# Optimization experiments

Measured on AMD Instinct MI355X. Metric: run time of the kernel, lower is better.

Reference implementation:

```python
import jax, jax.numpy as jnp
import numpy as np

NEG = -10000.0
MAX_SPAN_LEN = 30
TOP_LAMBDA = 0.4
NUM_CATS = 7
FFNN = 1024
HID = 1024
B, S = 2, 2048
MAX_K = int(S * TOP_LAMBDA)  # 819; static top-k size (input_masks are full)


def fc(x, W, b, g, beta):
    # FullyConnectedLayer: Linear -> GELU(exact) -> LayerNorm (dropout = identity in eval)
    h = jax.nn.gelu(x @ W.T + b, approximate=False)
    mu = jnp.mean(h, axis=-1, keepdims=True)
    var = jnp.var(h, axis=-1, keepdims=True)
    return (h - mu) / jnp.sqrt(var + 1e-5) * g + beta


def setup_inputs():
    key = jax.random.key(0)
    ks = iter(jax.random.split(key, 48))
    def rn(shape, scale=0.02):
        return jax.random.normal(next(ks), shape, jnp.float32) * scale
    NF = NUM_CATS * FFNN
    inp = {
        'input_emb': jax.random.normal(next(ks), (B, S, HID), jnp.float32),
        'input_masks': jnp.ones((B, S), jnp.int32),
        # start/end mention MLPs
        'sm_W': rn((FFNN, HID)), 'sm_b': jnp.zeros((FFNN,)), 'sm_g': jnp.ones((FFNN,)), 'sm_beta': jnp.zeros((FFNN,)),
        'em_W': rn((FFNN, HID)), 'em_b': jnp.zeros((FFNN,)), 'em_g': jnp.ones((FFNN,)), 'em_beta': jnp.zeros((FFNN,)),
        # mention start/end classifiers (Linear(F,1)) and s2e classifier
        'ms_w': rn((FFNN,)), 'ms_b': jnp.zeros(()),
        'me_w': rn((FFNN,)), 'me_b': jnp.zeros(()),
        's2e_W': rn((FFNN, FFNN)), 's2e_b': jnp.zeros((FFNN,)),
        # coref start/end all-category MLPs (output num_cats*ffnn)
        'cs_W': rn((NF, HID)), 'cs_b': jnp.zeros((NF,)), 'cs_g': jnp.ones((NF,)), 'cs_beta': jnp.zeros((NF,)),
        'ce_W': rn((NF, HID)), 'ce_b': jnp.zeros((NF,)), 'ce_g': jnp.ones((NF,)), 'ce_beta': jnp.zeros((NF,)),
        # per-category bilinear antecedent weights/biases
        'Ws2s': rn((NUM_CATS, FFNN, FFNN)), 'We2e': rn((NUM_CATS, FFNN, FFNN)),
        'Ws2e': rn((NUM_CATS, FFNN, FFNN)), 'We2s': rn((NUM_CATS, FFNN, FFNN)),
        'Bs2s': rn((NUM_CATS, FFNN)), 'Be2e': rn((NUM_CATS, FFNN)),
        'Bs2e': rn((NUM_CATS, FFNN)), 'Be2s': rn((NUM_CATS, FFNN)),
    }
    return inp


def reference(input_emb, input_masks, sm_W, sm_b, sm_g, sm_beta, em_W, em_b, em_g, em_beta,
              ms_w, ms_b, me_w, me_b, s2e_W, s2e_b, cs_W, cs_b, cs_g, cs_beta,
              ce_W, ce_b, ce_g, ce_beta, Ws2s, We2e, Ws2e, We2s, Bs2s, Be2e, Bs2e, Be2s):
    # --- mention scores ---
    s = fc(input_emb, sm_W, sm_b, sm_g, sm_beta)   # [B,S,F]
    e = fc(input_emb, em_W, em_b, em_g, em_beta)   # [B,S,F]
    sm = s @ ms_w + ms_b                            # [B,S]
    em = e @ me_w + me_b                            # [B,S]
    joint = jnp.einsum('bsf,btf->bst', s @ s2e_W.T + s2e_b, e)
    scores = joint + sm[:, :, None] + em[:, None, :]
    i = jnp.arange(S)
    band = ((i[None, :] >= i[:, None]) & (i[None, :] - i[:, None] < MAX_SPAN_LEN)).astype(scores.dtype)
    scores = scores + (1.0 - band) * NEG            # mask_tensor (additive)
    # --- top-k span pruning ---
    flat = scores.reshape(B, S * S)
    _, idx = jax.lax.top_k(flat, MAX_K)
    k = (jnp.sum(input_masks, axis=-1).astype(jnp.float32) * TOP_LAMBDA).astype(jnp.int32)
    span_mask = (jnp.arange(MAX_K)[None, :] < k[:, None]).astype(jnp.int32)  # [B,K]
    idx = idx * span_mask + (1 - span_mask) * (S * S - 1)
    idx = jnp.sort(idx, axis=-1)
    start_ids = idx // S
    end_ids = idx % S
    topk_scores = jnp.take_along_axis(flat, idx, axis=1)          # [B,K]
    pair_scores = topk_scores[:, :, None] + topk_scores[:, None, :]
    # --- per-category coref reps (gather then MLP) ---
    start_reps = jnp.take_along_axis(input_emb, start_ids[:, :, None], axis=1)  # [B,K,H]
    end_reps = jnp.take_along_axis(input_emb, end_ids[:, :, None], axis=1)
    a_s = fc(start_reps, cs_W, cs_b, cs_g, cs_beta).reshape(B, MAX_K, NUM_CATS, FFNN).transpose(0, 2, 1, 3)
    a_e = fc(end_reps, ce_W, ce_b, ce_g, ce_beta).reshape(B, MAX_K, NUM_CATS, FFNN).transpose(0, 2, 1, 3)
    # --- per-category bilinear antecedent scores ---
    def bil(x, W, y):
        return jnp.einsum('bnkf,nfg,bnlg->bnkl', x, W, y)
    logits = bil(a_s, Ws2s, a_s) + bil(a_e, We2e, a_e) + bil(a_s, Ws2e, a_e) + bil(a_e, We2s, a_s)
    biases = (jnp.einsum('bnkf,nf->bnk', a_s, Bs2s) + jnp.einsum('bnkf,nf->bnk', a_e, Be2e)
              + jnp.einsum('bnkf,nf->bnk', a_e, Bs2e) + jnp.einsum('bnkf,nf->bnk', a_s, Be2s))[:, :, None, :]
    coref = logits + biases                                        # [B,N,K,K]
    kk = jnp.arange(MAX_K)
    tril = (kk[None, :] < kk[:, None]).astype(coref.dtype)         # strictly-lower (diag=-1)
    mask = tril[None, None] * span_mask[:, None, None, :].astype(coref.dtype)
    coref = coref + (1.0 - mask) * NEG
    return coref + pair_scores[:, None]
```

## Files before the change

kernel.cpp:

```cpp
#include <hip/hip_runtime.h>
#include <hip/hip_bf16.h>
#include <math.h>

#define S_    2048
#define NC_   7
#define MAXK  819
#define NK    1024
#define KP    896
#define Z_    14
#define NEGV  (-10000.0f)

typedef __attribute__((ext_vector_type(8))) short bf16x8;
typedef __attribute__((ext_vector_type(4))) float f32x4;

#define CFENCE asm volatile("" ::: "memory")
#define BAR    do { CFENCE; __builtin_amdgcn_s_barrier(); CFENCE; } while (0)

__device__ __forceinline__ void gload_lds16(const void* g, void* l) {
  __builtin_amdgcn_global_load_lds((const __attribute__((address_space(1))) unsigned int*)g,
                                   (__attribute__((address_space(3))) unsigned int*)l, 16, 0, 0);
}

__device__ __forceinline__ float gelu_exact(float x) {
  return 0.5f * x * (1.0f + erff(x * 0.70710678118654752f));
}
__device__ __forceinline__ unsigned short f2bf(float x) {
  __hip_bfloat16 h = __float2bfloat16(x);
  return *(unsigned short*)&h;
}
__device__ __forceinline__ float bf2f(unsigned short u) {
  __hip_bfloat16 h; *(unsigned short*)&h = u;
  return __bfloat162float(h);
}

template<bool OBF16, int EPI, bool MERGE>
__global__ __launch_bounds__(512, 2) void k_gemm8(
    const __hip_bfloat16* __restrict__ A, const __hip_bfloat16* __restrict__ B,
    void* __restrict__ Cv, const float* __restrict__ bias1, const float* __restrict__ bias2,
    const float* __restrict__ tkv, const int* __restrict__ kvp,
    int K, int nbn, long strideA, long strideB, int bmod7, long strideC,
    int ldc, int Mstore, int Nstore)
{
  __shared__ __align__(16) char lds[2][65536];
  const int tid = threadIdx.x;
  const int z = blockIdx.z;
  const int nwg = gridDim.x;
  const int xcd = blockIdx.x & 7, loc = blockIdx.x >> 3;
  const int q = nwg >> 3, r = nwg & 7;
  const int wg = (xcd < r ? xcd * (q + 1) : r * (q + 1) + (xcd - r) * q) + loc;
  const int bm = wg / nbn, bn = wg % nbn;
  const int m0 = bm * 256, n0 = bn * 256;
  const __hip_bfloat16* pA = A + (long)z * strideA;
  const __hip_bfloat16* pB = B + (long)(bmod7 ? (z % 7) : z) * strideB;
  const int wave = tid >> 6, lane = tid & 63;
  const int wm = wave >> 2, wn = wave & 3;
  const int lr = lane & 15, kh = lane >> 4;
  const long Kb = (long)K * 2;

  f32x4 acc[8][4];
  #pragma unroll
  for (int i = 0; i < 8; ++i)
    #pragma unroll
    for (int j = 0; j < 4; ++j)
      #pragma unroll
      for (int rr = 0; rr < 4; ++rr) acc[i][j][rr] = 0.0f;

  auto stageHalf = [&](int bb, int isB, int rh, int kt) {
    const long kbyte = (long)kt * 128;
    const char* basep;
    if (isB) {
      basep = (const char*)pB + (long)(n0 + rh * 128) * Kb;
    } else if (MERGE) {
      int arow0 = m0 + rh * 128;
      int zb = (arow0 >= KP) ? 1 : 0;
      basep = (const char*)(A + (long)(z + NC_ * zb) * strideA)
              + (long)(arow0 - KP * zb) * Kb;
    } else {
      basep = (const char*)pA + (long)(m0 + rh * 128) * Kb;
    }
    #pragma unroll
    for (int j = 0; j < 2; ++j) {
      int off = j * 8192 + tid * 16;
      int row = off >> 7;
      int col = off & 127;
      int gc = col ^ (((rh * 128 + row) & 7) << 4);
      gload_lds16(basep + (long)row * Kb + kbyte + gc,
                  &lds[bb][isB * 32768 + (rh * 128 + row) * 128 + col]);
    }
  };
  auto readA = [&](int c, int g, int kk) -> bf16x8 {
    int row = wm * 128 + g * 16 + lr;
    int colb = kk * 64 + kh * 16;
    return *(const bf16x8*)&lds[c][row * 128 + (colb ^ ((row & 7) << 4))];
  };
  auto readB = [&](int c, int ni, int kk) -> bf16x8 {
    int row = wn * 64 + ni * 16 + lr;
    int colb = kk * 64 + kh * 16;
    return *(const bf16x8*)&lds[c][32768 + row * 128 + (colb ^ ((row & 7) << 4))];
  };
  auto mfma4 = [&](int g0, bf16x8* af, bf16x8* bfr) {
    __builtin_amdgcn_s_setprio(1);
    #pragma unroll
    for (int mi = 0; mi < 4; ++mi)
      #pragma unroll
      for (int ni = 0; ni < 4; ++ni)
        acc[g0 + mi][ni] = __builtin_amdgcn_mfma_f32_16x16x32_bf16(af[mi], bfr[ni], acc[g0 + mi][ni], 0, 0, 0);
    __builtin_amdgcn_s_setprio(0);
  };

  const int nt = K >> 6;
  stageHalf(0, 1, 0, 0);
  stageHalf(0, 1, 1, 0);
  stageHalf(0, 0, 0, 0);
  stageHalf(0, 0, 1, 0);
  if (nt > 1) { stageHalf(1, 1, 0, 1); asm volatile("s_waitcnt vmcnt(2)" ::: "memory"); }
  else        { asm volatile("s_waitcnt vmcnt(0)" ::: "memory"); }
  BAR;
// ... 20 lines not shown
    #pragma unroll
    for (int i = 0; i < 4; ++i) a0f[i] = readA(c, i, 1);
    if (t + 1 < nt) stageHalf(cn, 0, 1, t + 1);
    BAR;
    mfma4(0, a0f, bfr);
    BAR;
    #pragma unroll
    for (int i = 0; i < 4; ++i) a1f[i] = readA(c, 4 + i, 1);
    if (t + 2 < nt) { stageHalf(c, 1, 0, t + 2); asm volatile("s_waitcnt vmcnt(2)" ::: "memory"); }
    else            { asm volatile("s_waitcnt vmcnt(0)" ::: "memory"); }
    BAR;
    mfma4(4, a1f, bfr);
    BAR;
  }

  const long coff = (long)z * strideC;
  int kval = 0, bb_ = 0;
  if (EPI == 2) { bb_ = z / NC_; kval = kvp[bb_]; }
  #pragma unroll
  for (int mi = 0; mi < 8; ++mi) {
    #pragma unroll
    for (int ni = 0; ni < 4; ++ni) {
      int n = n0 + wn * 64 + ni * 16 + lr;
      if (n >= Nstore) continue;
      float badd = 0.f;
      if (EPI == 0) { if (bias1) badd = bias1[n]; }
      if (EPI == 1) badd = (n >= 1024) ? bias2[n - 1024] : bias1[n];
      if (EPI == 2) badd = bias1[z * NK + n] + tkv[bb_ * NK + n];
      #pragma unroll
      for (int rr = 0; rr < 4; ++rr) {
        int m = m0 + wm * 128 + mi * 16 + kh * 4 + rr;
        if (m >= Mstore) continue;
        float v = acc[mi][ni][rr] + badd;
        long co; int mrow;
        if (MERGE) {
          int zb = (m >= KP) ? 1 : 0;
          co = (long)(z + NC_ * zb) * strideC;
          mrow = m - KP * zb;
        } else { co = coff; mrow = m; }
        if (EPI == 2) {
          v += tkv[bb_ * NK + m];
          if (!(n < m && n < kval)) v += NEGV;
        }
        if (OBF16) ((__hip_bfloat16*)Cv)[co + (long)mrow * ldc + n] = __float2bfloat16(v);
        else       ((float*)Cv)[co + (long)mrow * ldc + n] = v;
      }
    }
  }
}

template<int EPI>
__global__ __launch_bounds__(512, 1) void k_gemm44(
    const __hip_bfloat16* __restrict__ A, const __hip_bfloat16* __restrict__ B,
    float* __restrict__ Cv, const float* __restrict__ bias1, const float* __restrict__ bias2,
    int K, int nbn, int ldc, int Mstore, int Nstore)
{
  __shared__ __align__(16) char lds[3][49152];
  const int tid = threadIdx.x;
  const int nwg = gridDim.x;
  const int xcd = blockIdx.x & 7, loc = blockIdx.x >> 3;
  const int q = nwg >> 3, r = nwg & 7;
  const int wg = (xcd < r ? xcd * (q + 1) : r * (q + 1) + (xcd - r) * q) + loc;
  const int bm = wg / nbn, bn = wg % nbn;
  const int m0 = bm * 128, n0 = bn * 256;
  const int wave = tid >> 6, lane = tid & 63;
  const int wm = wave >> 2, wn = wave & 3;
  const int lr = lane & 15, kh = lane >> 4;
  const long Kb = (long)K * 2;

  f32x4 acc[4][4];
  #pragma unroll
  for (int i = 0; i < 4; ++i)
    #pragma unroll
    for (int j = 0; j < 4; ++j)
      #pragma unroll
      for (int rr = 0; rr < 4; ++rr) acc[i][j][rr] = 0.0f;

  auto stageA = [&](int bb, int kt) {
    const long kbyte = (long)kt * 128;
    const char* basep = (const char*)A + (long)m0 * Kb;
    #pragma unroll
    for (int j = 0; j < 2; ++j) {
      int off = j * 8192 + tid * 16;
      int row = off >> 7, col = off & 127;
      int gc = col ^ ((row & 7) << 4);
      gload_lds16(basep + (long)row * Kb + kbyte + gc, &lds[bb][row * 128 + col]);
    }
  };
  auto stageB = [&](int bb, int kt, int rh) {
    const long kbyte = (long)kt * 128;
    const char* basep = (const char*)B + (long)(n0 + rh * 128) * Kb;
    #pragma unroll
    for (int j = 0; j < 2; ++j) {
      int off = j * 8192 + tid * 16;
      int row = off >> 7, col = off & 127;
      int gc = col ^ (((rh * 128 + row) & 7) << 4);
      gload_lds16(basep + (long)row * Kb + kbyte + gc,
                  &lds[bb][16384 + (rh * 128 + row) * 128 + col]);
    }
  };
  auto readA = [&](int c, int g, int kk) -> bf16x8 {
    int row = wm * 64 + g * 16 + lr;
    int colb = kk * 64 + kh * 16;
    return *(const bf16x8*)&lds[c][row * 128 + (colb ^ ((row & 7) << 4))];
  };
  auto readB = [&](int c, int ni, int kk) -> bf16x8 {
    int row = wn * 64 + ni * 16 + lr;
    int colb = kk * 64 + kh * 16;
    return *(const bf16x8*)&lds[c][16384 + row * 128 + (colb ^ ((row & 7) << 4))];
  };
  auto mfmaAll = [&](bf16x8* af, bf16x8* bfr) {
    __builtin_amdgcn_s_setprio(1);
    #pragma unroll
    for (int mi = 0; mi < 4; ++mi)
      #pragma unroll
      for (int ni = 0; ni < 4; ++ni)
        acc[mi][ni] = __builtin_amdgcn_mfma_f32_16x16x32_bf16(af[mi], bfr[ni], acc[mi][ni], 0, 0, 0);
    __builtin_amdgcn_s_setprio(0);
  };

  const int nt = K >> 6;
  stageA(0, 0); stageB(0, 0, 0); stageB(0, 0, 1);
  if (nt > 1) { stageA(1, 1); stageB(1, 1, 0); stageB(1, 1, 1);
                asm volatile("s_waitcnt vmcnt(6)" ::: "memory"); }
  else        { asm volatile("s_waitcnt vmcnt(0)" ::: "memory"); }
  BAR;

  bf16x8 af[4], bfr[4];
  int ct = 0;
  for (int t = 0; t < nt; ++t) {
    const int b2 = (ct + 2 >= 3) ? ct - 1 : ct + 2;
    #pragma unroll
    for (int i = 0; i < 4; ++i) bfr[i] = readB(ct, i, 0);
    #pragma unroll
    for (int i = 0; i < 4; ++i) af[i] = readA(ct, i, 0);
    if (t + 2 < nt) stageA(b2, t + 2);
    BAR;
    mfmaAll(af, bfr);
    BAR;
    #pragma unroll
    for (int i = 0; i < 4; ++i) bfr[i] = readB(ct, i, 1);
    #pragma unroll
    for (int i = 0; i < 4; ++i) af[i] = readA(ct, i, 1);
    if (t + 2 < nt) { stageB(b2, t + 2, 0); stageB(b2, t + 2, 1);
                      asm volatile("s_waitcnt vmcnt(6)" ::: "memory"); }
    else            { asm volatile("s_waitcnt vmcnt(0)" ::: "memory"); }
    BAR;
    mfmaAll(af, bfr);
    BAR;
    ct = (ct + 1 >= 3) ? 0 : ct + 1;
  }

  #pragma unroll
  for (int mi = 0; mi < 4; ++mi) {
    #pragma unroll
    for (int ni = 0; ni < 4; ++ni) {
      int n = n0 + wn * 64 + ni * 16 + lr;
      if (n >= Nstore) continue;
      float badd = 0.f;
      if (EPI == 0) { if (bias1) badd = bias1[n]; }
      if (EPI == 1) badd = (n >= 1024) ? bias2[n - 1024] : bias1[n];
      #pragma unroll
      for (int rr = 0; rr < 4; ++rr) {
        int m = m0 + wm * 64 + mi * 16 + kh * 4 + rr;
        if (m >= Mstore) continue;
        Cv[(long)m * ldc + n] = acc[mi][ni][rr] + badd;
      }
    }
  }
}

template<bool APAT>
__global__ __launch_bounds__(256) void k_packsplit3(const float* __restrict__ s1, long stride1,
                                                    const float* __restrict__ s2, int split,
                                                    __hip_bfloat16* __restrict__ dst) {
  long idx4 = ((long)blockIdx.x * 256 + threadIdx.x) * 4;
  int rrow = (int)(idx4 >> 10), c = (int)(idx4 & 1023);
  const float* src = (rrow < split) ? s1 + (long)rrow * stride1 + c
                                    : s2 + (long)(rrow - split) * 1024 + c;
  float4 v = *(const float4*)src;
  float f[4] = {v.x, v.y, v.z, v.w};
  unsigned short h[4], l4[4];
  #pragma unroll
  for (int i = 0; i < 4; ++i) {
    h[i] = f2bf(f[i]);
    l4[i] = f2bf(f[i] - bf2f(h[i]));
  }
  unsigned short* d = (unsigned short*)dst + (long)rrow * 3072;
  ushort4 hv = {h[0], h[1], h[2], h[3]};
  ushort4 lv = {l4[0], l4[1], l4[2], l4[3]};
// ... 1 lines not shown
  *(ushort4*)(d + 1024 + c) = APAT ? hv : lv;
  *(ushort4*)(d + 2048 + c) = APAT ? lv : hv;
}

__global__ __launch_bounds__(256) void k_cast4(const float* __restrict__ x,
                                               __hip_bfloat16* __restrict__ y, long n4) {
  long i = (long)blockIdx.x * 256 + threadIdx.x;
  if (i >= n4) return;
  float4 v = ((const float4*)x)[i];
  ushort4 o = {f2bf(v.x), f2bf(v.y), f2bf(v.z), f2bf(v.w)};
  ((ushort4*)y)[i] = o;
}

__global__ __launch_bounds__(256) void k_packBbig(const float* __restrict__ Ws2s,
                                                  const float* __restrict__ We2e,
                                                  const float* __restrict__ Ws2e,
                                                  const float* __restrict__ We2s,
                                                  __hip_bfloat16* __restrict__ dst) {
  long idx4 = ((long)blockIdx.x * 256 + threadIdx.x) * 4;
  long rowid = idx4 >> 11;
  int c = (int)(idx4 & 2047);
  int cat = (int)(rowid >> 11);
  int n = (int)(rowid & 2047);
  const float* src;
  if (n < 1024) src = (c < 1024) ? Ws2s + ((long)cat * 1024 + n) * 1024 + c
                                 : Ws2e + ((long)cat * 1024 + n) * 1024 + (c - 1024);
  else          src = (c < 1024) ? We2s + ((long)cat * 1024 + (n - 1024)) * 1024 + c
                                 : We2e + ((long)cat * 1024 + (n - 1024)) * 1024 + (c - 1024);
  float4 v = *(const float4*)src;
  ushort4 o = {f2bf(v.x), f2bf(v.y), f2bf(v.z), f2bf(v.w)};
  *(ushort4*)((unsigned short*)dst + idx4) = o;
}

__global__ __launch_bounds__(256) void k_ln_s(const float* __restrict__ se,
                                              const float* __restrict__ g,
                                              const float* __restrict__ beta,
                                              const float* __restrict__ wv,
                                              const float* __restrict__ b0,
                                              float* __restrict__ smv,
                                              __hip_bfloat16* __restrict__ ssp) {
  int r = blockIdx.x;
  int c4 = threadIdx.x;
  float4 x = ((const float4*)(se + (long)r * 2048))[c4];
  float v[4] = {gelu_exact(x.x), gelu_exact(x.y), gelu_exact(x.z), gelu_exact(x.w)};
  float s = v[0] + v[1] + v[2] + v[3];
  float s2 = v[0]*v[0] + v[1]*v[1] + v[2]*v[2] + v[3]*v[3];
  __shared__ float red0[4], red1[4];
  for (int off = 32; off; off >>= 1) { s += __shfl_xor(s, off); s2 += __shfl_xor(s2, off); }
  int w = threadIdx.x >> 6;
  if ((threadIdx.x & 63) == 0) { red0[w] = s; red1[w] = s2; }
  __syncthreads();
  s  = red0[0] + red0[1] + red0[2] + red0[3];
  s2 = red1[0] + red1[1] + red1[2] + red1[3];
  float mu  = s / 1024.0f;
  float var = s2 / 1024.0f - mu * mu;
  float inv = 1.0f / sqrtf(var + 1e-5f);
  float4 gg = ((const float4*)g)[c4], bb = ((const float4*)beta)[c4];
  float y[4] = {(v[0]-mu)*inv*gg.x + bb.x, (v[1]-mu)*inv*gg.y + bb.y,
                (v[2]-mu)*inv*gg.z + bb.z, (v[3]-mu)*inv*gg.w + bb.w};
  float4 w4 = ((const float4*)wv)[c4];
  float d = y[0]*w4.x + y[1]*w4.y + y[2]*w4.z + y[3]*w4.w;
  for (int off = 32; off; off >>= 1) d += __shfl_xor(d, off);
  __syncthreads();
  if ((threadIdx.x & 63) == 0) red0[w] = d;
  __syncthreads();
  if (threadIdx.x == 0)
    smv[r] = red0[0] + red0[1] + red0[2] + red0[3] + b0[0];
  unsigned short h[4], l4[4];
  #pragma unroll
  for (int i = 0; i < 4; ++i) { h[i] = f2bf(y[i]); l4[i] = f2bf(y[i] - bf2f(h[i])); }
  ushort4 hv = {h[0], h[1], h[2], h[3]};
  ushort4 lv = {l4[0], l4[1], l4[2], l4[3]};
  unsigned short* dst = (unsigned short*)ssp + (long)r * 3072 + c4 * 4;
  *(ushort4*)dst          = hv;
  *(ushort4*)(dst + 1024) = hv;
  *(ushort4*)(dst + 2048) = lv;
}

__global__ __launch_bounds__(256) void k_ln_e(float* __restrict__ se,
                                              const float* __restrict__ g,
                                              const float* __restrict__ beta,
                                              const float* __restrict__ wv,
                                              const float* __restrict__ b0,
                                              float* __restrict__ emv) {
  int r = blockIdx.x;
  int c4 = threadIdx.x;
  float4* rowp = (float4*)(se + (long)r * 2048 + 1024);
  float4 x = rowp[c4];
  float v[4] = {gelu_exact(x.x), gelu_exact(x.y), gelu_exact(x.z), gelu_exact(x.w)};
  float s = v[0] + v[1] + v[2] + v[3];
  float s2 = v[0]*v[0] + v[1]*v[1] + v[2]*v[2] + v[3]*v[3];
  __shared__ float red0[4], red1[4];
  for (int off = 32; off; off >>= 1) { s += __shfl_xor(s, off); s2 += __shfl_xor(s2, off); }
  int w = threadIdx.x >> 6;
  if ((threadIdx.x & 63) == 0) { red0[w] = s; red1[w] = s2; }
  __syncthreads();
  s  = red0[0] + red0[1] + red0[2] + red0[3];
  s2 = red1[0] + red1[1] + red1[2] + red1[3];
  float mu  = s / 1024.0f;
  float var = s2 / 1024.0f - mu * mu;
  float inv = 1.0f / sqrtf(var + 1e-5f);
  float4 gg = ((const float4*)g)[c4], bb = ((const float4*)beta)[c4];
  float4 y = {(v[0]-mu)*inv*gg.x + bb.x, (v[1]-mu)*inv*gg.y + bb.y,
              (v[2]-mu)*inv*gg.z + bb.z, (v[3]-mu)*inv*gg.w + bb.w};
  float4 w4 = ((const float4*)wv)[c4];
  float d = y.x*w4.x + y.y*w4.y + y.z*w4.z + y.w*w4.w;
  for (int off = 32; off; off >>= 1) d += __shfl_xor(d, off);
  __syncthreads();
  if ((threadIdx.x & 63) == 0) red0[w] = d;
  __syncthreads();
  if (threadIdx.x == 0)
    emv[r] = red0[0] + red0[1] + red0[2] + red0[3] + b0[0];
  rowp[c4] = y;
}

__global__ __launch_bounds__(256) void k_gelu_ln_cats(const __hip_bfloat16* __restrict__ h,
                                                      const float* __restrict__ g,
                                                      const float* __restrict__ beta,
                                                      __hip_bfloat16* __restrict__ a_cat, int half) {
  int r = blockIdx.x;
  int b = (r >= KP) ? 1 : 0, k = r - KP * b;
  const ushort4* row = (const ushort4*)((const unsigned short*)h + (long)r * 7168);
  float v[28];
  float s = 0.f, s2 = 0.f;
  #pragma unroll
  for (int j = 0; j < 7; ++j) {
    ushort4 u = row[threadIdx.x + 256 * j];
    #pragma unroll
    for (int e = 0; e < 4; ++e) {
      float x = bf2f(((const unsigned short*)&u)[e]);
      float ge = gelu_exact(x);
      v[j * 4 + e] = ge; s += ge; s2 += ge * ge;
    }
  }
  __shared__ float red0[4], red1[4];
  for (int off = 32; off; off >>= 1) { s += __shfl_xor(s, off); s2 += __shfl_xor(s2, off); }
  int w = threadIdx.x >> 6;
  if ((threadIdx.x & 63) == 0) { red0[w] = s; red1[w] = s2; }
  __syncthreads();
  s  = red0[0] + red0[1] + red0[2] + red0[3];
  s2 = red1[0] + red1[1] + red1[2] + red1[3];
  float mu  = s / 7168.0f;
  float var = s2 / 7168.0f - mu * mu;
  float inv = 1.0f / sqrtf(var + 1e-5f);
  #pragma unroll
  for (int j = 0; j < 7; ++j) {
// ... 26 lines not shown
  for (int qq = 0; qq < 16; ++qq) sreg[qq] = sp[l + 64 * qq];
  float myS = smv[(b << 11) + s];
  if (l < 32) {
    int j = l;
    if (j >= 30 || s + j >= S_)
      band[((long)(b << 11) + s) * 32 + j] = -3.0e38f;
  }
  {
    const float* ep = se + ((long)(b << 11) + s0) * 2048 + 1024;
    ebuf[0][tid * 2]     = ep[tid * 2];
    ebuf[0][tid * 2 + 1] = ep[tid * 2 + 1];
  }
  for (int it = 0; it < 37; ++it) {
    int t = s0 + it;
    __syncthreads();
    if (it + 1 < 37 && s0 + it + 1 < S_) {
      const float* ep = se + ((long)(b << 11) + s0 + it + 1) * 2048 + 1024;
      ebuf[(it + 1) & 1][tid * 2]     = ep[tid * 2];
      ebuf[(it + 1) & 1][tid * 2 + 1] = ep[tid * 2 + 1];
    }
    int j = t - s;
    if (t < S_ && j >= 0 && j < 30) {
      const float* eb = ebuf[it & 1];
      float acc = 0.f;
      #pragma unroll
      for (int qq = 0; qq < 16; ++qq) acc += sreg[qq] * eb[l + 64 * qq];
      for (int off = 32; off; off >>= 1) acc += __shfl_xor(acc, off);
      if (l == 0)
        band[((long)(b << 11) + s) * 32 + j] = acc + myS + emv[(b << 11) + t];
    }
  }
}

__device__ __forceinline__ void bitonic1024(unsigned* buf) {
  int tid = threadIdx.x;
  __syncthreads();
  for (int k = 2; k <= 1024; k <<= 1)
    for (int j = k >> 1; j > 0; j >>= 1) {
      int ixj = tid ^ j;
      if (ixj > tid) {
        unsigned a = buf[tid], c = buf[ixj];
        bool up = ((tid & k) == 0);
        if (up ? (a > c) : (a < c)) { buf[tid] = c; buf[ixj] = a; }
      }
      __syncthreads();
    }
}

__global__ __launch_bounds__(1024) void k_topk(const float* __restrict__ band,
                                               const int* __restrict__ masks,
                                               int* __restrict__ starts, int* __restrict__ ends,
                                               float* __restrict__ tk, int* __restrict__ kvalid_out) {
  int b = blockIdx.x;
  const float* bb = band + (long)b * 65536;
  __shared__ unsigned hist[16][256];
  __shared__ int sh_digit, sh_R, sh_msum;
  __shared__ unsigned cntG, cntE;
  __shared__ unsigned listG[832];
  __shared__ unsigned listE[1024];
  __shared__ unsigned buf[1024];
  int tid = threadIdx.x;
  int wv = tid >> 6;

  if (tid == 0) sh_msum = 0;
  __syncthreads();
  int pm = masks[b * S_ + tid] + masks[b * S_ + 1024 + tid];
  atomicAdd(&sh_msum, pm);
  __syncthreads();
  int kv = (int)((float)sh_msum * 0.4f);
  if (kv > MAXK) kv = MAXK;

  unsigned prefix = 0;
  int R = kv;
  if (kv > 0) {
    for (int shift = 24; shift >= 0; shift -= 8) {
      for (int i = tid; i < 4096; i += 1024) ((unsigned*)hist)[i] = 0;
      __syncthreads();
      for (int i = tid; i < 65536; i += 1024) {
        unsigned u = __float_as_uint(bb[i]);
        unsigned key = (u & 0x80000000u) ? ~u : (u | 0x80000000u);
        bool ok = (shift == 24) || ((key >> (shift + 8)) == (prefix >> (shift + 8)));
        if (ok) atomicAdd(&hist[wv][(key >> shift) & 255u], 1u);
      }
      __syncthreads();
      if (tid < 256) {
        unsigned sacc = 0;
        #pragma unroll
        for (int ww = 0; ww < 16; ++ww) sacc += hist[ww][tid];
        hist[0][tid] = sacc;
      }
      __syncthreads();
      if (tid == 0) {
        unsigned cum = 0; int d;
        for (d = 255; d >= 0; --d) {
          unsigned hc = hist[0][d];
          if (cum + hc >= (unsigned)R) break;
          cum += hc;
        }
        if (d < 0) d = 0;
        sh_digit = d; sh_R = R - (int)cum;
      }
      __syncthreads();
      prefix |= ((unsigned)sh_digit) << shift;
      R = sh_R;
      __syncthreads();
    }
  }
  if (tid == 0) { cntG = 0; cntE = 0; }
  __syncthreads();
  if (kv > 0) {
    for (int i = tid; i < 65536; i += 1024) {
      unsigned u = __float_as_uint(bb[i]);
      unsigned key = (u & 0x80000000u) ? ~u : (u | 0x80000000u);
      if (key > prefix) { unsigned p = atomicAdd(&cntG, 1u); if (p < 832) listG[p] = (unsigned)i; }
      else if (key == prefix) { unsigned p = atomicAdd(&cntE, 1u); if (p < 1024) listE[p] = (unsigned)i; }
    }
  }
  __syncthreads();
  int nG = (int)cntG, nE = (int)cntE, need = R;
  buf[tid] = (tid < nE) ? listE[tid] : 0xFFFFFFFFu;
  bitonic1024(buf);
  if (tid < need) listG[nG + tid] = buf[tid];
  __syncthreads();
  unsigned v2 = (tid < (unsigned)kv) ? listG[tid] : 0xFFFFFFFFu;
  __syncthreads();
  buf[tid] = v2;
  bitonic1024(buf);
  {
    int s, t; float val;
    if (tid < kv) {
      unsigned i = buf[tid];
      s = (int)(i >> 5); t = s + (int)(i & 31);
      val = bb[i];
    } else {
      s = S_ - 1; t = S_ - 1;
      val = bb[(S_ - 1) * 32 + 0];
    }
    starts[b * NK + tid] = s;
    ends[b * NK + tid] = t;
    tk[b * NK + tid] = val;
  }
  if (tid == 0) kvalid_out[b] = kv;
}

__global__ __launch_bounds__(256) void k_gather(const float* __restrict__ emb,
                                                const int* __restrict__ starts,
                                                const int* __restrict__ ends,
                                                __hip_bfloat16* __restrict__ reps_s,
// ... 67 lines not shown
  const float* Ws2s = (const float*)d_in[24];
  const float* We2e = (const float*)d_in[25];
  const float* Ws2e = (const float*)d_in[26];
  const float* We2s = (const float*)d_in[27];
  const float* Bs2s = (const float*)d_in[28];
  const float* Be2e = (const float*)d_in[29];
  const float* Bs2e = (const float*)d_in[30];
  const float* Be2s = (const float*)d_in[31];
  float* outp = (float*)d_out;
  char* ws = (char*)d_ws;
  (void)in_sizes; (void)n_in; (void)out_size; (void)ws_size;

  const size_t o_embsp = 0;
  const size_t o_bse   = 25165824;
  const size_t o_ssp   = 0;
  const size_t o_s2W   = 25165824;
  const size_t o_repss = 0;
  const size_t o_repse = 4194304;
  const size_t o_csWb  = 8388608;
  const size_t o_ceWb  = 23068672;
  const size_t o_Bbig  = 0;
  const size_t o_se    = 37748736;
  const size_t o_s2    = 71303168;
  const size_t o_h     = 88080384;
  const size_t o_acat  = 146800640;
  const size_t o_smv   = 205520896;
  const size_t o_emv   = o_smv + 16384;
  const size_t o_band  = o_emv + 16384;
  const size_t o_starts= o_band + 524288;
  const size_t o_ends  = o_starts + 8192;
  const size_t o_tk    = o_ends + 8192;
  const size_t o_kv    = o_tk + 8192;
  const size_t o_biasv = o_kv + 256;

  __hip_bfloat16* embsp = (__hip_bfloat16*)(ws + o_embsp);
  __hip_bfloat16* bse   = (__hip_bfloat16*)(ws + o_bse);
  __hip_bfloat16* ssp   = (__hip_bfloat16*)(ws + o_ssp);
  __hip_bfloat16* s2Wsp = (__hip_bfloat16*)(ws + o_s2W);
  __hip_bfloat16* repss = (__hip_bfloat16*)(ws + o_repss);
  __hip_bfloat16* repse = (__hip_bfloat16*)(ws + o_repse);
  __hip_bfloat16* csWb  = (__hip_bfloat16*)(ws + o_csWb);
  __hip_bfloat16* ceWb  = (__hip_bfloat16*)(ws + o_ceWb);
  __hip_bfloat16* Bbig  = (__hip_bfloat16*)(ws + o_Bbig);
  float* se_buf = (float*)(ws + o_se);
  float* s2_buf = (float*)(ws + o_s2);
  __hip_bfloat16* h_buf = (__hip_bfloat16*)(ws + o_h);
  __hip_bfloat16* Vcat  = (__hip_bfloat16*)(ws + o_h);
  __hip_bfloat16* a_cat = (__hip_bfloat16*)(ws + o_acat);
  float* smv_p = (float*)(ws + o_smv);
  float* emv_p = (float*)(ws + o_emv);
  float* band_p = (float*)(ws + o_band);
  int* starts_p = (int*)(ws + o_starts);
  int* ends_p = (int*)(ws + o_ends);
  float* tk_p = (float*)(ws + o_tk);
  int* kv_p = (int*)(ws + o_kv);
  float* biasv_p = (float*)(ws + o_biasv);

  k_packsplit3<true ><<<4096, 256, 0, stream>>>(x_emb, 1024, x_emb, 4096, embsp);
  k_packsplit3<false><<<2048, 256, 0, stream>>>(smW, 1024, emW, 1024, bse);
  k_gemm44<1><<<dim3(256, 1, 1), 512, 0, stream>>>(embsp, bse, se_buf, smb, embb,
      3072, 8, 2048, 4096, 2048);
  k_ln_s<<<4096, 256, 0, stream>>>(se_buf, smg, smbe, msw, msb, smv_p, ssp);
  k_ln_e<<<4096, 256, 0, stream>>>(se_buf, emg, embe, mew, meb, emv_p);

  k_packsplit3<false><<<1024, 256, 0, stream>>>(s2eW, 1024, s2eW, 1024, s2Wsp);
  k_gemm44<0><<<dim3(128, 1, 1), 512, 0, stream>>>(ssp, s2Wsp, s2_buf, s2eb, nullptr,
      3072, 4, 1024, 4096, 1024);
  k_band<<<512, 512, 0, stream>>>(s2_buf, se_buf, smv_p, emv_p, band_p);

  k_topk<<<2, 1024, 0, stream>>>(band_p, masks, starts_p, ends_p, tk_p, kv_p);

  k_gather<<<2 * KP, 256, 0, stream>>>(x_emb, starts_p, ends_p, repss, repse);
  k_cast4<<<7168, 256, 0, stream>>>(csW, csWb, 1835008);
  k_cast4<<<7168, 256, 0, stream>>>(ceW, ceWb, 1835008);
  k_gemm8<true, 0, false><<<dim3(196, 1, 1), 512, 0, stream>>>(repss, csWb, h_buf, csb, nullptr,
      nullptr, nullptr, 1024, 28, 0, 0, 0, 0, 7168, 2 * KP, 7168);
  k_gelu_ln_cats<<<2 * KP, 256, 0, stream>>>(h_buf, csg, csbe, a_cat, 0);
  k_gemm8<true, 0, false><<<dim3(196, 1, 1), 512, 0, stream>>>(repse, ceWb, h_buf, ceb, nullptr,
      nullptr, nullptr, 1024, 28, 0, 0, 0, 0, 7168, 2 * KP, 7168);
  k_packBbig<<<28672, 256, 0, stream>>>(Ws2s, We2e, Ws2e, We2s, Bbig);
  k_gelu_ln_cats<<<2 * KP, 256, 0, stream>>>(h_buf, ceg, cebe, a_cat, 1);

  k_gemm8<true, 0, true><<<dim3(56, 1, NC_), 512, 0, stream>>>(a_cat, Bbig, Vcat, nullptr, nullptr,
      nullptr, nullptr, 2048, 8, (long)NK * 2048, (long)2048 * 2048, 0, (long)NK * 2048, 2048, 2 * KP, 2048);
  k_bias<<<(Z_ * KP) / 4, 256, 0, stream>>>(a_cat, Bs2s, Be2e, Bs2e, Be2s, biasv_p);
  k_gemm8<false, 2, false><<<dim3(16, 1, Z_), 512, 0, stream>>>(a_cat, Vcat, outp, biasv_p, nullptr,
      tk_p, kv_p, 2048, 4, (long)NK * 2048, (long)NK * 2048, 0, (long)MAXK * MAXK, MAXK, MAXK, MAXK);
}
```

Measured before the change: 747.9 us.

## Parallelize top-k selection, fuse start/end layernorms, retile s2e GEMM

Replaces the two-block radix top-k with a multi-block pipeline. A global histogram on the top 12 bits finds a threshold bin, a collect pass keeps only candidate indices, and the final radix refinement runs on that much smaller set. It also fuses the start and end LayerNorm kernels into one launch and gives the s2e GEMM a 128-wide N tile so it launches 256 workgroups. The merged-batch path of k_gemm8 is removed, and the V GEMM now runs per batch over z=14 padded to 1024 rows, which does extra work on padded rows. The new top-k adds several small launches and global atomics.

```diff
diff --git a/kernel.cpp b/kernel.cpp
--- a/kernel.cpp
+++ b/kernel.cpp
@@ -32,8 +32,12 @@
   __hip_bfloat16 h; *(unsigned short*)&h = u;
   return __bfloat162float(h);
 }
-
-template<bool OBF16, int EPI, bool MERGE>
+__device__ __forceinline__ unsigned fkey(float f) {
+  unsigned u = __float_as_uint(f);
+  return (u & 0x80000000u) ? ~u : (u | 0x80000000u);
+}
+
+template<bool OBF16, int EPI>
 __global__ __launch_bounds__(512, 2) void k_gemm8(
     const __hip_bfloat16* __restrict__ A, const __hip_bfloat16* __restrict__ B,
     void* __restrict__ Cv, const float* __restrict__ bias1, const float* __restrict__ bias2,
@@ -67,22 +71,12 @@
 
   auto stageHalf = [&](int bb, int isB, int rh, int kt) {
     const long kbyte = (long)kt * 128;
-    const char* basep;
-    if (isB) {
-      basep = (const char*)pB + (long)(n0 + rh * 128) * Kb;
-    } else if (MERGE) {
-      int arow0 = m0 + rh * 128;
-      int zb = (arow0 >= KP) ? 1 : 0;
-      basep = (const char*)(A + (long)(z + NC_ * zb) * strideA)
-              + (long)(arow0 - KP * zb) * Kb;
-    } else {
-      basep = (const char*)pA + (long)(m0 + rh * 128) * Kb;
-    }
+    const char* basep = isB ? (const char*)pB + (long)(n0 + rh * 128) * Kb
+                            : (const char*)pA + (long)(m0 + rh * 128) * Kb;
     #pragma unroll
     for (int j = 0; j < 2; ++j) {
       int off = j * 8192 + tid * 16;
-      int row = off >> 7;
-      int col = off & 127;
+      int row = off >> 7, col = off & 127;
       int gc = col ^ (((rh * 128 + row) & 7) << 4);
       gload_lds16(basep + (long)row * Kb + kbyte + gc,
                   &lds[bb][isB * 32768 + (rh * 128 + row) * 128 + col]);
@@ -169,47 +163,43 @@
         int m = m0 + wm * 128 + mi * 16 + kh * 4 + rr;
         if (m >= Mstore) continue;
         float v = acc[mi][ni][rr] + badd;
-        long co; int mrow;
-        if (MERGE) {
-          int zb = (m >= KP) ? 1 : 0;
-          co = (long)(z + NC_ * zb) * strideC;
-          mrow = m - KP * zb;
-        } else { co = coff; mrow = m; }
         if (EPI == 2) {
           v += tkv[bb_ * NK + m];
           if (!(n < m && n < kval)) v += NEGV;
         }
-        if (OBF16) ((__hip_bfloat16*)Cv)[co + (long)mrow * ldc + n] = __float2bfloat16(v);
-        else       ((float*)Cv)[co + (long)mrow * ldc + n] = v;
+        if (OBF16) ((__hip_bfloat16*)Cv)[coff + (long)m * ldc + n] = __float2bfloat16(v);
+        else       ((float*)Cv)[coff + (long)m * ldc + n] = v;
       }
     }
   }
 }
 
-template<int EPI>
+template<int EPI, int BN>
 __global__ __launch_bounds__(512, 1) void k_gemm44(
     const __hip_bfloat16* __restrict__ A, const __hip_bfloat16* __restrict__ B,
     float* __restrict__ Cv, const float* __restrict__ bias1, const float* __restrict__ bias2,
     int K, int nbn, int ldc, int Mstore, int Nstore)
 {
-  __shared__ __align__(16) char lds[3][49152];
+  constexpr int NI = BN / 64;
+  constexpr int NBH = BN / 128;
+  __shared__ __align__(16) char lds[3][16384 + BN * 128];
   const int tid = threadIdx.x;
   const int nwg = gridDim.x;
   const int xcd = blockIdx.x & 7, loc = blockIdx.x >> 3;
   const int q = nwg >> 3, r = nwg & 7;
   const int wg = (xcd < r ? xcd * (q + 1) : r * (q + 1) + (xcd - r) * q) + loc;
   const int bm = wg / nbn, bn = wg % nbn;
-  const int m0 = bm * 128, n0 = bn * 256;
+  const int m0 = bm * 128, n0 = bn * BN;
   const int wave = tid >> 6, lane = tid & 63;
   const int wm = wave >> 2, wn = wave & 3;
   const int lr = lane & 15, kh = lane >> 4;
   const long Kb = (long)K * 2;
 
-  f32x4 acc[4][4];
+  f32x4 acc[4][NI];
   #pragma unroll
   for (int i = 0; i < 4; ++i)
     #pragma unroll
-    for (int j = 0; j < 4; ++j)
+    for (int j = 0; j < NI; ++j)
       #pragma unroll
       for (int rr = 0; rr < 4; ++rr) acc[i][j][rr] = 0.0f;
 
@@ -242,7 +232,7 @@
     return *(const bf16x8*)&lds[c][row * 128 + (colb ^ ((row & 7) << 4))];
   };
   auto readB = [&](int c, int ni, int kk) -> bf16x8 {
-    int row = wn * 64 + ni * 16 + lr;
+    int row = wn * (NI * 16) + ni * 16 + lr;
     int colb = kk * 64 + kh * 16;
     return *(const bf16x8*)&lds[c][16384 + row * 128 + (colb ^ ((row & 7) << 4))];
   };
@@ -251,24 +241,32 @@
     #pragma unroll
     for (int mi = 0; mi < 4; ++mi)
       #pragma unroll
-      for (int ni = 0; ni < 4; ++ni)
+      for (int ni = 0; ni < NI; ++ni)
         acc[mi][ni] = __builtin_amdgcn_mfma_f32_16x16x32_bf16(af[mi], bfr[ni], acc[mi][ni], 0, 0, 0);
     __builtin_amdgcn_s_setprio(0);
   };
 
   const int nt = K >> 6;
-  stageA(0, 0); stageB(0, 0, 0); stageB(0, 0, 1);
-  if (nt > 1) { stageA(1, 1); stageB(1, 1, 0); stageB(1, 1, 1);
-                asm volatile("s_waitcnt vmcnt(6)" ::: "memory"); }
-  else        { asm volatile("s_waitcnt vmcnt(0)" ::: "memory"); }
+  stageA(0, 0);
+  #pragma unroll
+  for (int rh = 0; rh < NBH; ++rh) stageB(0, 0, rh);
+  if (nt > 1) {
+    stageA(1, 1);
+    #pragma unroll
+    for (int rh = 0; rh < NBH; ++rh) stageB(1, 1, rh);
+    if (BN == 256) asm volatile("s_waitcnt vmcnt(6)" ::: "memory");
+    else           asm volatile("s_waitcnt vmcnt(4)" ::: "memory");
+  } else {
+    asm volatile("s_waitcnt vmcnt(0)" ::: "memory");
+  }
   BAR;
 
-  bf16x8 af[4], bfr[4];
+  bf16x8 af[4], bfr[NI];
   int ct = 0;
   for (int t = 0; t < nt; ++t) {
     const int b2 = (ct + 2 >= 3) ? ct - 1 : ct + 2;
     #pragma unroll
-    for (int i = 0; i < 4; ++i) bfr[i] = readB(ct, i, 0);
+    for (int i = 0; i < NI; ++i) bfr[i] = readB(ct, i, 0);
     #pragma unroll
     for (int i = 0; i < 4; ++i) af[i] = readA(ct, i, 0);
     if (t + 2 < nt) stageA(b2, t + 2);
@@ -276,12 +274,17 @@
     mfmaAll(af, bfr);
     BAR;
     #pragma unroll
-    for (int i = 0; i < 4; ++i) bfr[i] = readB(ct, i, 1);
+    for (int i = 0; i < NI; ++i) bfr[i] = readB(ct, i, 1);
     #pragma unroll
     for (int i = 0; i < 4; ++i) af[i] = readA(ct, i, 1);
-    if (t + 2 < nt) { stageB(b2, t + 2, 0); stageB(b2, t + 2, 1);
-                      asm volatile("s_waitcnt vmcnt(6)" ::: "memory"); }
-    else            { asm volatile("s_waitcnt vmcnt(0)" ::: "memory"); }
+    if (t + 2 < nt) {
+      #pragma unroll
+      for (int rh = 0; rh < NBH; ++rh) stageB(b2, t + 2, rh);
+      if (BN == 256) asm volatile("s_waitcnt vmcnt(6)" ::: "memory");
+      else           asm volatile("s_waitcnt vmcnt(4)" ::: "memory");
+    } else {
+      asm volatile("s_waitcnt vmcnt(0)" ::: "memory");
+    }
     BAR;
     mfmaAll(af, bfr);
     BAR;
@@ -291,8 +294,8 @@
   #pragma unroll
   for (int mi = 0; mi < 4; ++mi) {
     #pragma unroll
-    for (int ni = 0; ni < 4; ++ni) {
-      int n = n0 + wn * 64 + ni * 16 + lr;
+    for (int ni = 0; ni < NI; ++ni) {
+      int n = n0 + wn * (NI * 16) + ni * 16 + lr;
       if (n >= Nstore) continue;
       float badd = 0.f;
       if (EPI == 0) { if (bias1) badd = bias1[n]; }
@@ -360,26 +363,32 @@
   *(ushort4*)((unsigned short*)dst + idx4) = o;
 }
 
-__global__ __launch_bounds__(256) void k_ln_s(const float* __restrict__ se,
-                                              const float* __restrict__ g,
-                                              const float* __restrict__ beta,
-                                              const float* __restrict__ wv,
-                                              const float* __restrict__ b0,
-                                              float* __restrict__ smv,
-                                              __hip_bfloat16* __restrict__ ssp) {
+__global__ __launch_bounds__(512) void k_ln_se(float* __restrict__ se,
+                                               const float* __restrict__ sg, const float* __restrict__ sbe,
+                                               const float* __restrict__ eg, const float* __restrict__ ebe,
+                                               const float* __restrict__ msw, const float* __restrict__ msb,
+                                               const float* __restrict__ mew, const float* __restrict__ meb,
+                                               float* __restrict__ smv, float* __restrict__ emv,
+                                               __hip_bfloat16* __restrict__ ssp) {
   int r = blockIdx.x;
-  int c4 = threadIdx.x;
-  float4 x = ((const float4*)(se + (long)r * 2048))[c4];
+  int tid = threadIdx.x;
+  int half = tid >> 8;
+  int c4 = tid & 255;
+  int w8 = tid >> 6;
+  const float* g    = half ? eg : sg;
+  const float* beta = half ? ebe : sbe;
+  const float* wv   = half ? mew : msw;
+  float4* rowp = (float4*)(se + (long)r * 2048 + half * 1024);
+  float4 x = rowp[c4];
   float v[4] = {gelu_exact(x.x), gelu_exact(x.y), gelu_exact(x.z), gelu_exact(x.w)};
   float s = v[0] + v[1] + v[2] + v[3];
   float s2 = v[0]*v[0] + v[1]*v[1] + v[2]*v[2] + v[3]*v[3];
-  __shared__ float red0[4], red1[4];
+  __shared__ float red0[8], red1[8];
   for (int off = 32; off; off >>= 1) { s += __shfl_xor(s, off); s2 += __shfl_xor(s2, off); }
-  int w = threadIdx.x >> 6;
-  if ((threadIdx.x & 63) == 0) { red0[w] = s; red1[w] = s2; }
-  __syncthreads();
-  s  = red0[0] + red0[1] + red0[2] + red0[3];
-  s2 = red1[0] + red1[1] + red1[2] + red1[3];
+  if ((tid & 63) == 0) { red0[w8] = s; red1[w8] = s2; }
+  __syncthreads();
+  s  = red0[half*4] + red0[half*4+1] + red0[half*4+2] + red0[half*4+3];
+  s2 = red1[half*4] + red1[half*4+1] + red1[half*4+2] + red1[half*4+3];
   float mu  = s / 1024.0f;
   float var = s2 / 1024.0f - mu * mu;
   float inv = 1.0f / sqrtf(var + 1e-5f);
@@ -390,56 +399,27 @@
   float d = y[0]*w4.x + y[1]*w4.y + y[2]*w4.z + y[3]*w4.w;
   for (int off = 32; off; off >>= 1) d += __shfl_xor(d, off);
   __syncthreads();
-  if ((threadIdx.x & 63) == 0) red0[w] = d;
-  __syncthreads();
-  if (threadIdx.x == 0)
-    smv[r] = red0[0] + red0[1] + red0[2] + red0[3] + b0[0];
-  unsigned short h[4], l4[4];
-  #pragma unroll
-  for (int i = 0; i < 4; ++i) { h[i] = f2bf(y[i]); l4[i] = f2bf(y[i] - bf2f(h[i])); }
-  ushort4 hv = {h[0], h[1], h[2], h[3]};
-  ushort4 lv = {l4[0], l4[1], l4[2], l4[3]};
-  unsigned short* dst = (unsigned short*)ssp + (long)r * 3072 + c4 * 4;
-  *(ushort4*)dst          = hv;
-  *(ushort4*)(dst + 1024) = hv;
-  *(ushort4*)(dst + 2048) = lv;
-}
-
-__global__ __launch_bounds__(256) void k_ln_e(float* __restrict__ se,
-                                              const float* __restrict__ g,
-                                              const float* __restrict__ beta,
-                                              const float* __restrict__ wv,
-                                              const float* __restrict__ b0,
-                                              float* __restrict__ emv) {
-  int r = blockIdx.x;
-  int c4 = threadIdx.x;
-  float4* rowp = (float4*)(se + (long)r * 2048 + 1024);
-  float4 x = rowp[c4];
-  float v[4] = {gelu_exact(x.x), gelu_exact(x.y), gelu_exact(x.z), gelu_exact(x.w)};
-  float s = v[0] + v[1] + v[2] + v[3];
-  float s2 = v[0]*v[0] + v[1]*v[1] + v[2]*v[2] + v[3]*v[3];
-  __shared__ float red0[4], red1[4];
-  for (int off = 32; off; off >>= 1) { s += __shfl_xor(s, off); s2 += __shfl_xor(s2, off); }
-  int w = threadIdx.x >> 6;
-  if ((threadIdx.x & 63) == 0) { red0[w] = s; red1[w] = s2; }
-  __syncthreads();
-  s  = red0[0] + red0[1] + red0[2] + red0[3];
-  s2 = red1[0] + red1[1] + red1[2] + red1[3];
-  float mu  = s / 1024.0f;
-  float var = s2 / 1024.0f - mu * mu;
-  float inv = 1.0f / sqrtf(var + 1e-5f);
-  float4 gg = ((const float4*)g)[c4], bb = ((const float4*)beta)[c4];
-  float4 y = {(v[0]-mu)*inv*gg.x + bb.x, (v[1]-mu)*inv*gg.y + bb.y,
-              (v[2]-mu)*inv*gg.z + bb.z, (v[3]-mu)*inv*gg.w + bb.w};
-  float4 w4 = ((const float4*)wv)[c4];
-  float d = y.x*w4.x + y.y*w4.y + y.z*w4.z + y.w*w4.w;
-  for (int off = 32; off; off >>= 1) d += __shfl_xor(d, off);
-  __syncthreads();
-  if ((threadIdx.x & 63) == 0) red0[w] = d;
-  __syncthreads();
-  if (threadIdx.x == 0)
-    emv[r] = red0[0] + red0[1] + red0[2] + red0[3] + b0[0];
-  rowp[c4] = y;
+  if ((tid & 63) == 0) red0[w8] = d;
+  __syncthreads();
+  if ((tid & 255) == 0) {
+    float dv = red0[half*4] + red0[half*4+1] + red0[half*4+2] + red0[half*4+3];
+    if (half == 0) smv[r] = dv + msb[0];
+    else           emv[r] = dv + meb[0];
+  }
+  if (half == 0) {
+    unsigned short h[4], l4[4];
+    #pragma unroll
+    for (int i = 0; i < 4; ++i) { h[i] = f2bf(y[i]); l4[i] = f2bf(y[i] - bf2f(h[i])); }
+    ushort4 hv = {h[0], h[1], h[2], h[3]};
+    ushort4 lv = {l4[0], l4[1], l4[2], l4[3]};
+    unsigned short* dst = (unsigned short*)ssp + (long)r * 3072 + c4 * 4;
+    *(ushort4*)dst          = hv;
+    *(ushort4*)(dst + 1024) = hv;
+    *(ushort4*)(dst + 2048) = lv;
+  } else {
+    float4 yo = {y[0], y[1], y[2], y[3]};
+    rowp[c4] = yo;
+  }
 }
 
 __global__ __launch_bounds__(256) void k_gelu_ln_cats(const __hip_bfloat16* __restrict__ h,
@@ -532,6 +512,103 @@
   }
 }
 
+__global__ __launch_bounds__(1024) void k_tkzero(unsigned* __restrict__ ghist,
+                                                 unsigned* __restrict__ gcnt) {
+  int i = blockIdx.x * 1024 + threadIdx.x;
+  if (i < 2 * 4096) ghist[i] = 0;
+  if (i < 2) gcnt[i] = 0;
+}
+
+__global__ __launch_bounds__(1024) void k_tkhist(const float* __restrict__ band,
+                                                 unsigned* __restrict__ ghist) {
+  int b = blockIdx.y;
+  const float* bb = band + (long)b * 65536;
+  __shared__ unsigned lh[4096];
+  int tid = threadIdx.x;
+  #pragma unroll
+  for (int j = 0; j < 4; ++j) lh[tid + j * 1024] = 0;
+  __syncthreads();
+  int base = blockIdx.x * 4096;
+  #pragma unroll
+  for (int j = 0; j < 4; ++j) {
+    unsigned key = fkey(bb[base + tid + j * 1024]);
+    atomicAdd(&lh[key >> 20], 1u);
+  }
+  __syncthreads();
+  #pragma unroll
+  for (int j = 0; j < 4; ++j) {
+    unsigned v = lh[tid + j * 1024];
+    if (v) atomicAdd(&ghist[b * 4096 + tid + j * 1024], v);
+  }
+}
+
+__global__ __launch_bounds__(1024) void k_tkscan(const unsigned* __restrict__ ghist,
+                                                 const int* __restrict__ masks,
+                                                 unsigned* __restrict__ sel) {
+  int b = blockIdx.x;
+  int tid = threadIdx.x;
+  __shared__ unsigned cs[1024];
+  __shared__ int red[16];
+  __shared__ int sh_kv;
+  int pm = masks[b * S_ + tid] + masks[b * S_ + 1024 + tid];
+  for (int off = 32; off; off >>= 1) pm += __shfl_xor(pm, off);
+  if ((tid & 63) == 0) red[tid >> 6] = pm;
+  __syncthreads();
+  if (tid == 0) {
+    int msum = 0;
+    for (int i = 0; i < 16; ++i) msum += red[i];
+    int kv = (int)((float)msum * 0.4f);
+    if (kv > MAXK) kv = MAXK;
+    sh_kv = kv;
+  }
+  __syncthreads();
+  int kv = sh_kv;
+  unsigned hbin[4];
+  unsigned ssum = 0;
+  #pragma unroll
+  for (int j = 0; j < 4; ++j) { hbin[j] = ghist[b * 4096 + tid * 4 + j]; ssum += hbin[j]; }
+  cs[tid] = ssum;
+  __syncthreads();
+  for (int off = 1; off < 1024; off <<= 1) {
+    unsigned add = (tid + off < 1024) ? cs[tid + off] : 0u;
+    __syncthreads();
+    cs[tid] += add;
+    __syncthreads();
+  }
+  unsigned above = cs[tid] - ssum;
+  if (kv > 0) {
+    unsigned aa = above;
+    for (int j = 3; j >= 0; --j) {
+      if (aa < (unsigned)kv && aa + hbin[j] >= (unsigned)kv) sel[b * 2] = (unsigned)(tid * 4 + j);
+      aa += hbin[j];
+    }
+  }
+  if (tid == 0) {
+    sel[b * 2 + 1] = (unsigned)kv;
+    if (kv == 0) sel[b * 2] = 0xFFFFFFFFu;
+  }
+}
+
+__global__ __launch_bounds__(1024) void k_tkcollect(const float* __restrict__ band,
+                                                    const unsigned* __restrict__ sel,
+                                                    unsigned* __restrict__ cand,
+                                                    unsigned* __restrict__ gcnt) {
+  int b = blockIdx.y;
+  const float* bb = band + (long)b * 65536;
+  unsigned thr = sel[b * 2];
+  int base = blockIdx.x * 4096;
+  int tid = threadIdx.x;
+  #pragma unroll
+  for (int j = 0; j < 4; ++j) {
+    int i = base + tid + j * 1024;
+    unsigned key = fkey(bb[i]);
+    if ((key >> 20) >= thr) {
+      unsigned p = atomicAdd(&gcnt[b], 1u);
+      cand[(long)b * 65536 + p] = (unsigned)i;
+    }
+  }
+}
+
 __device__ __forceinline__ void bitonic1024(unsigned* buf) {
   int tid = threadIdx.x;
   __syncthreads();
@@ -547,53 +624,41 @@
     }
 }
 
-__global__ __launch_bounds__(1024) void k_topk(const float* __restrict__ band,
-                                               const int* __restrict__ masks,
-                                               int* __restrict__ starts, int* __restrict__ ends,
-                                               float* __restrict__ tk, int* __restrict__ kvalid_out) {
+__global__ __launch_bounds__(1024) void k_tkfinal(const float* __restrict__ band,
+                                                  const unsigned* __restrict__ cand,
+                                                  const unsigned* __restrict__ gcnt,
+                                                  const unsigned* __restrict__ sel,
+                                                  int* __restrict__ starts, int* __restrict__ ends,
+                                                  float* __restrict__ tk, int* __restrict__ kvalid_out) {
   int b = blockIdx.x;
   const float* bb = band + (long)b * 65536;
-  __shared__ unsigned hist[16][256];
-  __shared__ int sh_digit, sh_R, sh_msum;
+  const unsigned* cd = cand + (long)b * 65536;
+  int nC = (int)gcnt[b];
+  int kv = (int)sel[b * 2 + 1];
+  __shared__ unsigned hist[256];
+  __shared__ int sh_digit, sh_R;
   __shared__ unsigned cntG, cntE;
   __shared__ unsigned listG[832];
   __shared__ unsigned listE[1024];
   __shared__ unsigned buf[1024];
   int tid = threadIdx.x;
-  int wv = tid >> 6;
-
-  if (tid == 0) sh_msum = 0;
-  __syncthreads();
-  int pm = masks[b * S_ + tid] + masks[b * S_ + 1024 + tid];
-  atomicAdd(&sh_msum, pm);
-  __syncthreads();
-  int kv = (int)((float)sh_msum * 0.4f);
-  if (kv > MAXK) kv = MAXK;
 
   unsigned prefix = 0;
   int R = kv;
   if (kv > 0) {
     for (int shift = 24; shift >= 0; shift -= 8) {
-      for (int i = tid; i < 4096; i += 1024) ((unsigned*)hist)[i] = 0;
+      if (tid < 256) hist[tid] = 0;
       __syncthreads();
-      for (int i = tid; i < 65536; i += 1024) {
-        unsigned u = __float_as_uint(bb[i]);
-        unsigned key = (u & 0x80000000u) ? ~u : (u | 0x80000000u);
+      for (int j = tid; j < nC; j += 1024) {
+        unsigned key = fkey(bb[cd[j]]);
         bool ok = (shift == 24) || ((key >> (shift + 8)) == (prefix >> (shift + 8)));
-        if (ok) atomicAdd(&hist[wv][(key >> shift) & 255u], 1u);
-      }
-      __syncthreads();
-      if (tid < 256) {
-        unsigned sacc = 0;
-        #pragma unroll
-        for (int ww = 0; ww < 16; ++ww) sacc += hist[ww][tid];
-        hist[0][tid] = sacc;
+        if (ok) atomicAdd(&hist[(key >> shift) & 255u], 1u);
       }
       __syncthreads();
       if (tid == 0) {
         unsigned cum = 0; int d;
         for (d = 255; d >= 0; --d) {
-          unsigned hc = hist[0][d];
+          unsigned hc = hist[d];
           if (cum + hc >= (unsigned)R) break;
           cum += hc;
         }
@@ -609,11 +674,11 @@
   if (tid == 0) { cntG = 0; cntE = 0; }
   __syncthreads();
   if (kv > 0) {
-    for (int i = tid; i < 65536; i += 1024) {
-      unsigned u = __float_as_uint(bb[i]);
-      unsigned key = (u & 0x80000000u) ? ~u : (u | 0x80000000u);
-      if (key > prefix) { unsigned p = atomicAdd(&cntG, 1u); if (p < 832) listG[p] = (unsigned)i; }
-      else if (key == prefix) { unsigned p = atomicAdd(&cntE, 1u); if (p < 1024) listE[p] = (unsigned)i; }
+    for (int j = tid; j < nC; j += 1024) {
+      unsigned i = cd[j];
+      unsigned key = fkey(bb[i]);
+      if (key > prefix) { unsigned p = atomicAdd(&cntG, 1u); if (p < 832) listG[p] = i; }
+      else if (key == prefix) { unsigned p = atomicAdd(&cntE, 1u); if (p < 1024) listE[p] = i; }
     }
   }
   __syncthreads();
@@ -747,6 +812,10 @@
   const size_t o_tk    = o_ends + 8192;
   const size_t o_kv    = o_tk + 8192;
   const size_t o_biasv = o_kv + 256;
+  const size_t o_ghist = o_biasv + 61440;
+  const size_t o_sel   = o_ghist + 32768;
+  const size_t o_gcnt  = o_sel + 256;
+  const size_t o_cand  = o_gcnt + 256;
 
   __hip_bfloat16* embsp = (__hip_bfloat16*)(ws + o_embsp);
   __hip_bfloat16* bse   = (__hip_bfloat16*)(ws + o_bse);
@@ -770,35 +839,44 @@
   float* tk_p = (float*)(ws + o_tk);
   int* kv_p = (int*)(ws + o_kv);
   float* biasv_p = (float*)(ws + o_biasv);
+  unsigned* ghist_p = (unsigned*)(ws + o_ghist);
+  unsigned* sel_p = (unsigned*)(ws + o_sel);
+  unsigned* gcnt_p = (unsigned*)(ws + o_gcnt);
+  unsigned* cand_p = (unsigned*)(ws + o_cand);
 
   k_packsplit3<true ><<<4096, 256, 0, stream>>>(x_emb, 1024, x_emb, 4096, embsp);
   k_packsplit3<false><<<2048, 256, 0, stream>>>(smW, 1024, emW, 1024, bse);
-  k_gemm44<1><<<dim3(256, 1, 1), 512, 0, stream>>>(embsp, bse, se_buf, smb, embb,
+  k_gemm44<1, 256><<<dim3(256, 1, 1), 512, 0, stream>>>(embsp, bse, se_buf, smb, embb,
       3072, 8, 2048, 4096, 2048);
-  k_ln_s<<<4096, 256, 0, stream>>>(se_buf, smg, smbe, msw, msb, smv_p, ssp);
-  k_ln_e<<<4096, 256, 0, stream>>>(se_buf, emg, embe, mew, meb, emv_p);
+  k_ln_se<<<4096, 512, 0, stream>>>(se_buf, smg, smbe, emg, embe, msw, msb, mew, meb,
+                                    smv_p, emv_p, ssp);
 
   k_packsplit3<false><<<1024, 256, 0, stream>>>(s2eW, 1024, s2eW, 1024, s2Wsp);
-  k_gemm44<0><<<dim3(128, 1, 1), 512, 0, stream>>>(ssp, s2Wsp, s2_buf, s2eb, nullptr,
-      3072, 4, 1024, 4096, 1024);
+  k_gemm44<0, 128><<<dim3(256, 1, 1), 512, 0, stream>>>(ssp, s2Wsp, s2_buf, s2eb, nullptr,
+      3072, 8, 1024, 4096, 1024);
   k_band<<<512, 512, 0, stream>>>(s2_buf, se_buf, smv_p, emv_p, band_p);
 
-  k_topk<<<2, 1024, 0, stream>>>(band_p, masks, starts_p, ends_p, tk_p, kv_p);
+  k_tkzero<<<9, 1024, 0, stream>>>(ghist_p, gcnt_p);
+  k_tkhist<<<dim3(16, 2), 1024, 0, stream>>>(band_p, ghist_p);
+  k_tkscan<<<2, 1024, 0, stream>>>(ghist_p, masks, sel_p);
+  k_tkcollect<<<dim3(16, 2), 1024, 0, stream>>>(band_p, sel_p, cand_p, gcnt_p);
+  k_tkfinal<<<2, 1024, 0, stream>>>(band_p, cand_p, gcnt_p, sel_p,
+                                    starts_p, ends_p, tk_p, kv_p);
 
   k_gather<<<2 * KP, 256, 0, stream>>>(x_emb, starts_p, ends_p, repss, repse);
   k_cast4<<<7168, 256, 0, stream>>>(csW, csWb, 1835008);
   k_cast4<<<7168, 256, 0, stream>>>(ceW, ceWb, 1835008);
-  k_gemm8<true, 0, false><<<dim3(196, 1, 1), 512, 0, stream>>>(repss, csWb, h_buf, csb, nullptr,
+  k_gemm8<true, 0><<<dim3(196, 1, 1), 512, 0, stream>>>(repss, csWb, h_buf, csb, nullptr,
       nullptr, nullptr, 1024, 28, 0, 0, 0, 0, 7168, 2 * KP, 7168);
   k_gelu_ln_cats<<<2 * KP, 256, 0, stream>>>(h_buf, csg, csbe, a_cat, 0);
-  k_gemm8<true, 0, false><<<dim3(196, 1, 1), 512, 0, stream>>>(repse, ceWb, h_buf, ceb, nullptr,
+  k_gemm8<true, 0><<<dim3(196, 1, 1), 512, 0, stream>>>(repse, ceWb, h_buf, ceb, nullptr,
       nullptr, nullptr, 1024, 28, 0, 0, 0, 0, 7168, 2 * KP, 7168);
   k_packBbig<<<28672, 256, 0, stream>>>(Ws2s, We2e, Ws2e, We2s, Bbig);
   k_gelu_ln_cats<<<2 * KP, 256, 0, stream>>>(h_buf, ceg, cebe, a_cat, 1);
 
-  k_gemm8<true, 0, true><<<dim3(56, 1, NC_), 512, 0, stream>>>(a_cat, Bbig, Vcat, nullptr, nullptr,
-      nullptr, nullptr, 2048, 8, (long)NK * 2048, (long)2048 * 2048, 0, (long)NK * 2048, 2048, 2 * KP, 2048);
+  k_gemm8<true, 0><<<dim3(32, 1, Z_), 512, 0, stream>>>(a_cat, Bbig, Vcat, nullptr, nullptr,
+      nullptr, nullptr, 2048, 8, (long)NK * 2048, (long)2048 * 2048, 1, (long)NK * 2048, 2048, NK, 2048);
   k_bias<<<(Z_ * KP) / 4, 256, 0, stream>>>(a_cat, Bs2s, Be2e, Bs2e, Be2s, biasv_p);
-  k_gemm8<false, 2, false><<<dim3(16, 1, Z_), 512, 0, stream>>>(a_cat, Vcat, outp, biasv_p, nullptr,
+  k_gemm8<false, 2><<<dim3(16, 1, Z_), 512, 0, stream>>>(a_cat, Vcat, outp, biasv_p, nullptr,
       tk_p, kv_p, 2048, 4, (long)NK * 2048, (long)NK * 2048, 0, (long)MAXK * MAXK, MAXK, MAXK, MAXK);
 }
```

After: 684.1 us. -8.5%, faster.
